# Kernel tuning notes

Hardware: AMD Instinct MI355X
Metric: run time of the kernel (lower is better)

## Reference

```python
import jax, jax.numpy as jnp
import numpy as np

# Module hyperparameters (from init_kwargs)
KH = KW = 3
STRIDE = 2
PAD = 1
OUT_PAD = 1
DIL = 1
IN_LEN = 8   # length of each input capsule
OUT_LEN = 8  # length of each output capsule
N_IN_CAPS = 64 // IN_LEN    # 8
N_OUT_CAPS = 64 // OUT_LEN  # 8
NUM_ITERATIONS = 3


def _squash(x):
    # v * |v|^2 / ((1 + |v|^2) * |v|), along last (capsule-length) dim
    sn = jnp.sum(x * x, axis=-1, keepdims=True)
    return x * (sn / ((1.0 + sn) * jnp.sqrt(sn + 1e-12)))


def _k_means_routing(priors, num_iterations):
    # priors: [..., K, M] ; soft k-means routing with 'dot' similarity,
    # softmax over the votes dim K (softmax_dim=-2), squash at the end.
    out = jnp.mean(priors, axis=-2, keepdims=True)          # [..., 1, M]
    for _ in range(num_iterations):
        nrm = jnp.linalg.norm(out, axis=-1, keepdims=True)
        out_n = out / jnp.maximum(nrm, 1e-12)               # F.normalize(p=2)
        logits = jnp.sum(priors * out_n, axis=-1, keepdims=True)  # [..., K, 1]
        probs = jax.nn.softmax(logits, axis=-2)
        out = jnp.sum(probs * priors, axis=-2, keepdims=True)
    return _squash(out)[..., 0, :]                          # [..., M]


def setup_inputs() -> dict:
    key = jax.random.key(0)
    k1, k2, k3 = jax.random.split(key, 3)
    input = jax.random.normal(k1, (2, 64, 32, 32), dtype=jnp.float32)
    # weight: (in_length, out_channels//out_length, out_length, kh, kw)
    weight = jax.random.normal(k2, (IN_LEN, N_OUT_CAPS, OUT_LEN, KH, KW), dtype=jnp.float32) * 0.1
    # bias: (out_channels//out_length, out_length)
    bias = jax.random.normal(k3, (N_OUT_CAPS, OUT_LEN), dtype=jnp.float32) * 0.1
    return {"input": input, "weight": weight, "bias": bias}


def reference(input, weight, bias):
    n, c_in, h_in, w_in = input.shape
    fi = c_in // IN_LEN
    fo = weight.shape[1]
    # conv_transpose == conv(lhs-dilated input, spatially flipped kernel)
    pad_lo = DIL * (KH - 1) - PAD
    patches = jax.lax.conv_general_dilated_patches(
        input, (KH, KW), (1, 1),
        padding=((pad_lo, pad_lo + OUT_PAD), (pad_lo, pad_lo + OUT_PAD)),
        lhs_dilation=(STRIDE, STRIDE), rhs_dilation=(DIL, DIL))
    ho, wo = patches.shape[-2], patches.shape[-1]
    # feature dim of patches is ordered (c, kh, kw), channel-major
    patches = patches.reshape(n, fi, IN_LEN, KH, KW, ho, wo)
    w_flip = weight[..., ::-1, ::-1]  # [IN_LEN, fo, OUT_LEN, KH, KW]
    # votes: each (input capsule, kernel tap) casts a vote per output capsule
    priors = jnp.einsum('nflhwpq,lgmhw->npqgfhwm', patches, w_flip)
    priors = priors.reshape(n, ho, wo, fo, fi * KH * KW, OUT_LEN)
    out = _k_means_routing(priors, NUM_ITERATIONS)  # [n, ho, wo, fo, OUT_LEN]
    out = out + bias                                # bias: [fo, OUT_LEN]
    out = out.reshape(n, ho, wo, fo * OUT_LEN).transpose(0, 3, 1, 2)
    return out  # [n, out_channels, ho, wo] = [2, 64, 64, 64]
```

## Files before the change

kernel.cpp:

```cpp
#include <hip/hip_runtime.h>
#include <math.h>

#define HIN 32
#define WIN 32
#define NITER 3

__global__ __launch_bounds__(256) void transpose_in(const float* __restrict__ in,
                                                    float* __restrict__ tin) {
    __shared__ float lds[64 * 33];
    const int t = threadIdx.x;
    const int n = blockIdx.x >> 5;
    const int s0 = (blockIdx.x & 31) << 5;
    const float* ib = in + n * 65536;
    float* ob = tin + n * 65536;
#pragma unroll
    for (int k = 0; k < 8; ++k) {
        int idx = k * 256 + t;
        int c = idx >> 5, sl = idx & 31;
        lds[c * 33 + sl] = ib[c * 1024 + s0 + sl];
    }
    __syncthreads();
#pragma unroll
    for (int k = 0; k < 8; ++k) {
        int idx = k * 256 + t;
        int sl = idx >> 6, c = idx & 63;
        ob[(size_t)(s0 + sl) * 64 + c] = lds[c * 33 + sl];
    }
}

template <int TH, int TW>
__device__ __forceinline__ void route_path(
    const float* __restrict__ tin,
    const float* __restrict__ wlds, const float* __restrict__ bias,
    float* __restrict__ olds,
    int n, int p, int q, int g, int s, int lane, int wave) {
    constexpr int T = TH * TW;
    constexpr float Z = (float)(72 - 8 * T);

    float pri[T][8];
#pragma unroll
    for (int i = 0; i < TH; ++i) {
        const int h = (TH == 1) ? 1 : i * 2;
        const int y = (p + h - 1) >> 1;
#pragma unroll
        for (int j = 0; j < TW; ++j) {
            const int w = (TW == 1) ? 1 : j * 2;
            const int x = (q + w - 1) >> 1;
            const int v = i * TW + j;
            const bool valid = (y < HIN) && (x < WIN);
            if (valid) {
                float xv[8];
                const float4* xp =
                    (const float4*)(tin + (((size_t)n * HIN + y) * WIN + x) * 64 + s * 8);
                float4 x0 = xp[0], x1 = xp[1];
                xv[0] = x0.x; xv[1] = x0.y; xv[2] = x0.z; xv[3] = x0.w;
                xv[4] = x1.x; xv[5] = x1.y; xv[6] = x1.z; xv[7] = x1.w;
                const int tap = h * 3 + w;
                const float* wb = wlds + (tap * 8 + g) * 64;
#pragma unroll
                for (int m = 0; m < 8; ++m) {
                    const float4* wp = (const float4*)(wb + ((m + g) & 7) * 8);
                    float4 w0 = wp[0], w1 = wp[1];
                    pri[v][m] = xv[0] * w0.x + xv[1] * w0.y + xv[2] * w0.z + xv[3] * w0.w +
                                xv[4] * w1.x + xv[5] * w1.y + xv[6] * w1.z + xv[7] * w1.w;
                }
            } else {
#pragma unroll
                for (int m = 0; m < 8; ++m) pri[v][m] = 0.f;
            }
        }
    }

    float o[8];
#pragma unroll
    for (int m = 0; m < 8; ++m) {
        float a = 0.f;
#pragma unroll
        for (int v = 0; v < T; ++v) a += pri[v][m];
        o[m] = a;
    }
#pragma unroll
    for (int st = 1; st <= 4; st <<= 1)
#pragma unroll
        for (int m = 0; m < 8; ++m) o[m] += __shfl_xor(o[m], st, 64);
#pragma unroll
    for (int m = 0; m < 8; ++m) o[m] *= (1.f / 72.f);

#pragma unroll
    for (int it = 0; it < NITER; ++it) {
        float sn = 0.f;
#pragma unroll
        for (int m = 0; m < 8; ++m) sn += o[m] * o[m];
        const float inv = __builtin_amdgcn_rsqf(fmaxf(sn, 1e-24f));
        float on[8];
#pragma unroll
        for (int m = 0; m < 8; ++m) on[m] = o[m] * inv;

        float e[T];
        float r[9];
        r[8] = 0.f;
#pragma unroll
        for (int v = 0; v < T; ++v) {
            float a = 0.f;
#pragma unroll
            for (int m = 0; m < 8; ++m) a += pri[v][m] * on[m];
            e[v] = __expf(a);
            r[8] += e[v];
        }
#pragma unroll
        for (int m = 0; m < 8; ++m) {
            float a = 0.f;
#pragma unroll
            for (int v = 0; v < T; ++v) a += e[v] * pri[v][m];
            r[m] = a;
        }
#pragma unroll
        for (int st = 1; st <= 4; st <<= 1)
#pragma unroll
            for (int j = 0; j < 9; ++j) r[j] += __shfl_xor(r[j], st, 64);
        const float invs = __builtin_amdgcn_rcpf(r[8] + Z);
#pragma unroll
        for (int m = 0; m < 8; ++m) o[m] = r[m] * invs;
    }

    float sn = 0.f;
#pragma unroll
    for (int m = 0; m < 8; ++m) sn += o[m] * o[m];
    const float factor =
        sn * __builtin_amdgcn_rcpf(1.f + sn) * __builtin_amdgcn_rsqf(sn + 1e-12f);

    float val = o[0];
#pragma unroll
    for (int m = 1; m < 8; ++m)
        if (s == m) val = o[m];
    val = val * factor + bias[g * 8 + s];

    olds[lane * 5 + wave] = val;
}

__global__ __launch_bounds__(256) void caps_routing(
    const float* __restrict__ tin, const float* __restrict__ weight,
    const float* __restrict__ bias, float* __restrict__ out) {
    __shared__ float wlds[4608];
    __shared__ float olds[64 * 5];
    const int t = threadIdx.x;

    {
        const int l = t & 7;
        const int g8 = (t >> 3) & 7;
        const int c = t >> 6;
        const float* wsrc = weight + ((l * 8 + g8) * 8 + c * 2) * 9;
        float* wd = wlds + g8 * 64 + l;
#pragma unroll
        for (int mi = 0; mi < 2; ++mi) {
            const int mg = ((c * 2 + mi + g8) & 7) * 8;
#pragma unroll
            for (int kh = 0; kh < 3; ++kh)
#pragma unroll
                for (int kw = 0; kw < 3; ++kw) {
                    const int tap = (2 - kh) * 3 + (2 - kw);
                    wd[tap * 512 + mg] = wsrc[mi * 9 + kh * 3 + kw];
                }
        }
    }
    __syncthreads();

    const int wave = t >> 6;
    const int lane = t & 63;
    const int g = lane >> 3;
    const int s = lane & 7;

    const int b = blockIdx.x;
    const int n = b >> 10;
    const int p = (b >> 4) & 63;
    const int j = b & 15;
    const int qpar = j >> 3;
    const int qb = (j & 7) * 8 + qpar;
    const int q = qb + 2 * wave;

    if (p & 1) {
        if (qpar)
            route_path<2, 2>(tin, wlds, bias, olds, n, p, q, g, s, lane, wave);
        else
            route_path<2, 1>(tin, wlds, bias, olds, n, p, q, g, s, lane, wave);
    } else {
        if (qpar)
            route_path<1, 2>(tin, wlds, bias, olds, n, p, q, g, s, lane, wave);
        else
            route_path<1, 1>(tin, wlds, bias, olds, n, p, q, g, s, lane, wave);
    }

    __syncthreads();
    const int c2 = t >> 2, w = t & 3;
    out[(((size_t)n * 64 + c2) * 64 + p) * 64 + qb + 2 * w] = olds[c2 * 5 + w];
}

extern "C" void kernel_launch(void* const* d_in, const int* in_sizes, int n_in,
                              void* d_out, int out_size, void* d_ws, size_t ws_size,
                              hipStream_t stream) {
    const float* in = (const float*)d_in[0];
    const float* weight = (const float*)d_in[1];
    const float* bias = (const float*)d_in[2];
    float* out = (float*)d_out;
    float* tin = (float*)d_ws;

    transpose_in<<<64, 256, 0, stream>>>(in, tin);
    caps_routing<<<2048, 256, 0, stream>>>(tin, weight, bias, out);
}
```

Before: 78.96 us.

## Give each thread two input capsules and reduce quads with DPP

Each thread now computes priors for two input capsules instead of one, which halves the number of lanes per output capsule. Cross-lane reductions shrink to a 4-lane DPP quad sum instead of 8-lane shfl_xor trees. Each block handles 8 output positions, so only half as many blocks are launched and the weight LDS staging is amortised over more work. Launch bounds now request 4 blocks per CU, and bias is added at store time. The cost is higher register pressure from the doubled prior array and less parallelism per block.

```diff
diff --git a/kernel.cpp b/kernel.cpp
--- a/kernel.cpp
+++ b/kernel.cpp
@@ -28,16 +28,25 @@
     }
 }
 
+template <int CTRL>
+__device__ __forceinline__ float qperm_add(float v) {
+    int p = __builtin_amdgcn_update_dpp(0, __float_as_int(v), CTRL, 0xF, 0xF, true);
+    return v + __int_as_float(p);
+}
+__device__ __forceinline__ float quad_sum(float v) {
+    v = qperm_add<0xB1>(v);
+    v = qperm_add<0x4E>(v);
+    return v;
+}
+
 template <int TH, int TW>
 __device__ __forceinline__ void route_path(
-    const float* __restrict__ tin,
-    const float* __restrict__ wlds, const float* __restrict__ bias,
-    float* __restrict__ olds,
-    int n, int p, int q, int g, int s, int lane, int wave) {
+    const float* __restrict__ tin, const float* __restrict__ wlds,
+    float* __restrict__ olds, int n, int p, int q, int g, int fs, int posidx) {
     constexpr int T = TH * TW;
     constexpr float Z = (float)(72 - 8 * T);
 
-    float pri[T][8];
+    float pri[2][T][8];
 #pragma unroll
     for (int i = 0; i < TH; ++i) {
         const int h = (TH == 1) ? 1 : i * 2;
@@ -49,24 +58,23 @@
             const int v = i * TW + j;
             const bool valid = (y < HIN) && (x < WIN);
             if (valid) {
-                float xv[8];
                 const float4* xp =
-                    (const float4*)(tin + (((size_t)n * HIN + y) * WIN + x) * 64 + s * 8);
-                float4 x0 = xp[0], x1 = xp[1];
-                xv[0] = x0.x; xv[1] = x0.y; xv[2] = x0.z; xv[3] = x0.w;
-                xv[4] = x1.x; xv[5] = x1.y; xv[6] = x1.z; xv[7] = x1.w;
+                    (const float4*)(tin + (((size_t)n * HIN + y) * WIN + x) * 64 + fs * 16);
+                float4 a0 = xp[0], a1 = xp[1], b0 = xp[2], b1 = xp[3];
                 const int tap = h * 3 + w;
                 const float* wb = wlds + (tap * 8 + g) * 64;
 #pragma unroll
                 for (int m = 0; m < 8; ++m) {
                     const float4* wp = (const float4*)(wb + ((m + g) & 7) * 8);
                     float4 w0 = wp[0], w1 = wp[1];
-                    pri[v][m] = xv[0] * w0.x + xv[1] * w0.y + xv[2] * w0.z + xv[3] * w0.w +
-                                xv[4] * w1.x + xv[5] * w1.y + xv[6] * w1.z + xv[7] * w1.w;
+                    pri[0][v][m] = a0.x * w0.x + a0.y * w0.y + a0.z * w0.z + a0.w * w0.w +
+                                   a1.x * w1.x + a1.y * w1.y + a1.z * w1.z + a1.w * w1.w;
+                    pri[1][v][m] = b0.x * w0.x + b0.y * w0.y + b0.z * w0.z + b0.w * w0.w +
+                                   b1.x * w1.x + b1.y * w1.y + b1.z * w1.z + b1.w * w1.w;
                 }
             } else {
 #pragma unroll
-                for (int m = 0; m < 8; ++m) pri[v][m] = 0.f;
+                for (int m = 0; m < 8; ++m) { pri[0][v][m] = 0.f; pri[1][v][m] = 0.f; }
             }
         }
     }
@@ -76,15 +84,9 @@
     for (int m = 0; m < 8; ++m) {
         float a = 0.f;
 #pragma unroll
-        for (int v = 0; v < T; ++v) a += pri[v][m];
-        o[m] = a;
-    }
-#pragma unroll
-    for (int st = 1; st <= 4; st <<= 1)
-#pragma unroll
-        for (int m = 0; m < 8; ++m) o[m] += __shfl_xor(o[m], st, 64);
-#pragma unroll
-    for (int m = 0; m < 8; ++m) o[m] *= (1.f / 72.f);
+        for (int v = 0; v < T; ++v) a += pri[0][v][m] + pri[1][v][m];
+        o[m] = quad_sum(a) * (1.f / 72.f);
+    }
 
 #pragma unroll
     for (int it = 0; it < NITER; ++it) {
@@ -96,28 +98,23 @@
 #pragma unroll
         for (int m = 0; m < 8; ++m) on[m] = o[m] * inv;
 
-        float e[T];
         float r[9];
-        r[8] = 0.f;
-#pragma unroll
-        for (int v = 0; v < T; ++v) {
-            float a = 0.f;
-#pragma unroll
-            for (int m = 0; m < 8; ++m) a += pri[v][m] * on[m];
-            e[v] = __expf(a);
-            r[8] += e[v];
-        }
-#pragma unroll
-        for (int m = 0; m < 8; ++m) {
-            float a = 0.f;
-#pragma unroll
-            for (int v = 0; v < T; ++v) a += e[v] * pri[v][m];
-            r[m] = a;
-        }
-#pragma unroll
-        for (int st = 1; st <= 4; st <<= 1)
-#pragma unroll
-            for (int j = 0; j < 9; ++j) r[j] += __shfl_xor(r[j], st, 64);
+#pragma unroll
+        for (int j = 0; j < 9; ++j) r[j] = 0.f;
+#pragma unroll
+        for (int f2 = 0; f2 < 2; ++f2)
+#pragma unroll
+            for (int v = 0; v < T; ++v) {
+                float a = 0.f;
+#pragma unroll
+                for (int m = 0; m < 8; ++m) a += pri[f2][v][m] * on[m];
+                const float e = __expf(a);
+                r[8] += e;
+#pragma unroll
+                for (int m = 0; m < 8; ++m) r[m] += e * pri[f2][v][m];
+            }
+#pragma unroll
+        for (int j = 0; j < 9; ++j) r[j] = quad_sum(r[j]);
         const float invs = __builtin_amdgcn_rcpf(r[8] + Z);
 #pragma unroll
         for (int m = 0; m < 8; ++m) o[m] = r[m] * invs;
@@ -129,20 +126,19 @@
     const float factor =
         sn * __builtin_amdgcn_rcpf(1.f + sn) * __builtin_amdgcn_rsqf(sn + 1e-12f);
 
-    float val = o[0];
-#pragma unroll
-    for (int m = 1; m < 8; ++m)
-        if (s == m) val = o[m];
-    val = val * factor + bias[g * 8 + s];
-
-    olds[lane * 5 + wave] = val;
-}
-
-__global__ __launch_bounds__(256) void caps_routing(
+    float v0 = o[0], v1 = o[4];
+#pragma unroll
+    for (int m = 1; m < 4; ++m)
+        if (fs == m) { v0 = o[m]; v1 = o[m + 4]; }
+    olds[(g * 8 + fs) * 9 + posidx] = v0 * factor;
+    olds[(g * 8 + fs + 4) * 9 + posidx] = v1 * factor;
+}
+
+__global__ __launch_bounds__(256, 4) void caps_routing(
     const float* __restrict__ tin, const float* __restrict__ weight,
     const float* __restrict__ bias, float* __restrict__ out) {
     __shared__ float wlds[4608];
-    __shared__ float olds[64 * 5];
+    __shared__ float olds[576];
     const int t = threadIdx.x;
 
     {
@@ -165,34 +161,36 @@
     }
     __syncthreads();
 
-    const int wave = t >> 6;
-    const int lane = t & 63;
-    const int g = lane >> 3;
-    const int s = lane & 7;
+    const int fs = t & 3;
+    const int g = (t >> 2) & 7;
+    const int posidx = ((t >> 6) << 1) | ((t >> 5) & 1);
 
     const int b = blockIdx.x;
-    const int n = b >> 10;
-    const int p = (b >> 4) & 63;
-    const int j = b & 15;
-    const int qpar = j >> 3;
-    const int qb = (j & 7) * 8 + qpar;
-    const int q = qb + 2 * wave;
+    const int n = b >> 9;
+    const int p = (b >> 3) & 63;
+    const int j = b & 7;
+    const int qpar = j >> 2;
+    const int qb = (j & 3) * 16 + qpar;
+    const int q = qb + 2 * posidx;
 
     if (p & 1) {
         if (qpar)
-            route_path<2, 2>(tin, wlds, bias, olds, n, p, q, g, s, lane, wave);
+            route_path<2, 2>(tin, wlds, olds, n, p, q, g, fs, posidx);
         else
-            route_path<2, 1>(tin, wlds, bias, olds, n, p, q, g, s, lane, wave);
+            route_path<2, 1>(tin, wlds, olds, n, p, q, g, fs, posidx);
     } else {
         if (qpar)
-            route_path<1, 2>(tin, wlds, bias, olds, n, p, q, g, s, lane, wave);
+            route_path<1, 2>(tin, wlds, olds, n, p, q, g, fs, posidx);
         else
-            route_path<1, 1>(tin, wlds, bias, olds, n, p, q, g, s, lane, wave);
+            route_path<1, 1>(tin, wlds, olds, n, p, q, g, fs, posidx);
     }
 
     __syncthreads();
-    const int c2 = t >> 2, w = t & 3;
-    out[(((size_t)n * 64 + c2) * 64 + p) * 64 + qb + 2 * w] = olds[c2 * 5 + w];
+    const int c = t >> 2, pi = t & 3;
+    const float bv = bias[c];
+    float* obase = out + (((size_t)n * 64 + c) * 64 + p) * 64 + qb;
+    obase[2 * pi] = olds[c * 9 + pi] + bv;
+    obase[2 * pi + 8] = olds[c * 9 + pi + 4] + bv;
 }
 
 extern "C" void kernel_launch(void* const* d_in, const int* in_sizes, int n_in,
@@ -205,5 +203,5 @@
     float* tin = (float*)d_ws;
 
     transpose_in<<<64, 256, 0, stream>>>(in, tin);
-    caps_routing<<<2048, 256, 0, stream>>>(tin, weight, bias, out);
-}
+    caps_routing<<<1024, 256, 0, stream>>>(tin, weight, bias, out);
+}
```

Result: slower. 85.30 us (+8.0%).
